# Kernel optimization log

Measured on AMD Instinct MI355X. Metric: run time of the kernel, lower is better.

## Reference

```python
import jax, jax.numpy as jnp
import numpy as np

DM = 1024
H = 16
DEPTH = DM // H


def setup_inputs() -> dict:
    key = jax.random.key(0)
    ks = jax.random.split(key, 11)
    B, S = 2, 2048
    scale = 1.0 / np.sqrt(DM)
    inp = {
        "Q": jax.random.normal(ks[0], (B, S, DM), dtype=jnp.float32),
        "K": jax.random.normal(ks[1], (B, S, DM), dtype=jnp.float32),
        "V": jax.random.normal(ks[2], (B, S, DM), dtype=jnp.float32),
        "Wq": jax.random.normal(ks[3], (DM, DM), dtype=jnp.float32) * scale,
        "bq": jnp.zeros((DM,), dtype=jnp.float32),
        "Wk": jax.random.normal(ks[4], (DM, DM), dtype=jnp.float32) * scale,
        "bk": jnp.zeros((DM,), dtype=jnp.float32),
        "Wv": jax.random.normal(ks[5], (DM, DM), dtype=jnp.float32) * scale,
        "bv": jnp.zeros((DM,), dtype=jnp.float32),
        "Wo": jax.random.normal(ks[6], (DM, DM), dtype=jnp.float32) * scale,
        "bo": jnp.zeros((DM,), dtype=jnp.float32),
    }
    return inp


def _split_heads(x, B):
    # [B, S, DM] -> [B, H, S, DEPTH]
    return x.reshape(B, -1, H, DEPTH).transpose(0, 2, 1, 3)


def reference(Q, K, V, Wq, bq, Wk, bk, Wv, bv, Wo, bo):
    B = Q.shape[0]
    q = _split_heads(Q @ Wq + bq, B)  # [B,H,S,D]
    k = _split_heads(K @ Wk + bk, B)
    v = _split_heads(V @ Wv + bv, B)
    logits = jnp.einsum("bhqd,bhkd->bhqk", q, k) / jnp.sqrt(
        jnp.asarray(DEPTH, dtype=q.dtype))
    weights = jax.nn.softmax(logits, axis=-1)  # [B,H,S,S]
    attn = jnp.einsum("bhqk,bhkd->bhqd", weights, v)
    concat = attn.transpose(0, 2, 1, 3).reshape(B, -1, DM)
    output = concat @ Wo + bo
    return output, weights
```

## Files before the change

kernel.cpp:

```cpp
#include <hip/hip_runtime.h>
#include <hip/hip_fp16.h>
#include <stdint.h>
#include <stddef.h>

typedef _Float16 f16;
typedef _Float16 f16x8 __attribute__((ext_vector_type(8)));
typedef _Float16 f16x4 __attribute__((ext_vector_type(4)));
typedef float    f32x4 __attribute__((ext_vector_type(4)));

#define NB  2
#define NS  2048
#define NDM 1024
#define NH  16
#define ND  64
#define NM  4096

__global__ __launch_bounds__(256) void cvt_x_kernel(const float* __restrict__ q,
                                                    const float* __restrict__ k,
                                                    const float* __restrict__ v,
                                                    f16* __restrict__ xh)
{
    const float* src = (blockIdx.y == 0) ? q : (blockIdx.y == 1) ? k : v;
    f16* dst = xh + (size_t)blockIdx.y * ((size_t)NM * NDM);
    size_t i = ((size_t)blockIdx.x * 256 + threadIdx.x) * 8;
    float4 a = *(const float4*)(src + i);
    float4 b = *(const float4*)(src + i + 4);
    f16x8 o;
    o[0] = (f16)a.x; o[1] = (f16)a.y; o[2] = (f16)a.z; o[3] = (f16)a.w;
    o[4] = (f16)b.x; o[5] = (f16)b.y; o[6] = (f16)b.z; o[7] = (f16)b.w;
    *(f16x8*)(dst + i) = o;
}

__global__ __launch_bounds__(256) void transp_w_kernel(const float* __restrict__ w0,
                                                       const float* __restrict__ w1,
                                                       const float* __restrict__ w2,
                                                       const float* __restrict__ w3,
                                                       f16* __restrict__ wt)
{
    __shared__ float t[64][65];
    const int z = blockIdx.z;
    const float* src = (z==0)?w0:(z==1)?w1:(z==2)?w2:w3;
    f16* dst = wt + (size_t)z * ((size_t)NDM * NDM);
    const int k0 = blockIdx.y * 64, n0 = blockIdx.x * 64;
    const int c = threadIdx.x & 63, r4 = threadIdx.x >> 6;
    #pragma unroll
    for (int i = 0; i < 16; ++i) {
        int r = i*4 + r4;
        t[r][c] = src[(size_t)(k0 + r) * NDM + n0 + c];
    }
    __syncthreads();
    #pragma unroll
    for (int i = 0; i < 16; ++i) {
        int n = i*4 + r4;
        dst[(size_t)(n0 + n) * NDM + k0 + c] = (f16)t[c][n];
    }
}

template<int MODE>
__device__ __forceinline__ void gemm128(const f16* __restrict__ A,
                                        const f16* __restrict__ Bw,
                                        const float* __restrict__ bias,
                                        void* __restrict__ outp,
                                        f16* __restrict__ AsB, f16* __restrict__ BsB)
{
    const int tid  = threadIdx.x;
    const int lane = tid & 63;
    const int wid  = tid >> 6;
    const int wr = wid >> 1, wc = wid & 1;
    const int m0 = blockIdx.y * 128, n0 = blockIdx.x * 128;
    const int K = 1024;

    const int r0 = tid >> 2;
    const int s0 = (tid & 3) * 8;
    const f16* Arow0 = A  + (size_t)(m0 + r0)      * K + s0;
    const f16* Arow1 = A  + (size_t)(m0 + r0 + 64) * K + s0;
    const f16* Brow0 = Bw + (size_t)(n0 + r0)      * K + s0;
    const f16* Brow1 = Bw + (size_t)(n0 + r0 + 64) * K + s0;
    const int lds0 = r0*32 + s0;
    const int lds1 = (r0+64)*32 + s0;

    f16x8 ra0 = *(const f16x8*)(Arow0);
    f16x8 ra1 = *(const f16x8*)(Arow1);
    f16x8 rb0 = *(const f16x8*)(Brow0);
    f16x8 rb1 = *(const f16x8*)(Brow1);
    *(f16x8*)(AsB + lds0) = ra0; *(f16x8*)(AsB + lds1) = ra1;
    *(f16x8*)(BsB + lds0) = rb0; *(f16x8*)(BsB + lds1) = rb1;

    f32x4 acc[4][4];
    #pragma unroll
    for (int i = 0; i < 4; ++i)
        #pragma unroll
        for (int j = 0; j < 4; ++j) {
            f32x4 z4 = {0.f, 0.f, 0.f, 0.f};
            acc[i][j] = z4;
        }

    const int arow = wr*64 + (lane & 15);
    const int brow = wc*64 + (lane & 15);
    const int kc   = (lane >> 4) * 8;

    int cur = 0;
    for (int s = 0; s < 32; ++s) {
        const bool more = (s + 1 < 32);
        if (more) {
            const int kk = (s + 1) * 32;
            ra0 = *(const f16x8*)(Arow0 + kk); ra1 = *(const f16x8*)(Arow1 + kk);
            rb0 = *(const f16x8*)(Brow0 + kk); rb1 = *(const f16x8*)(Brow1 + kk);
        }
        __syncthreads();
        {
            f16x8 af[4], bf[4];
            f16* Asc = AsB + cur*4096;
            f16* Bsc = BsB + cur*4096;
            #pragma unroll
            for (int rt = 0; rt < 4; ++rt) af[rt] = *(const f16x8*)(Asc + (arow + rt*16)*32 + kc);
            #pragma unroll
            for (int ct = 0; ct < 4; ++ct) bf[ct] = *(const f16x8*)(Bsc + (brow + ct*16)*32 + kc);
            #pragma unroll
            for (int rt = 0; rt < 4; ++rt)
                #pragma unroll
                for (int ct = 0; ct < 4; ++ct)
                    acc[rt][ct] = __builtin_amdgcn_mfma_f32_16x16x32_f16(af[rt], bf[ct], acc[rt][ct], 0, 0, 0);
        }
        __syncthreads();
        if (more) {
            f16* Asn = AsB + (cur^1)*4096;
            f16* Bsn = BsB + (cur^1)*4096;
            *(f16x8*)(Asn + lds0) = ra0; *(f16x8*)(Asn + lds1) = ra1;
            *(f16x8*)(Bsn + lds0) = rb0; *(f16x8*)(Bsn + lds1) = rb1;
        }
        cur ^= 1;
    }

    #pragma unroll
    for (int rt = 0; rt < 4; ++rt) {
        const int mb = m0 + wr*64 + rt*16 + ((lane >> 4) << 2);
        #pragma unroll
        for (int ct = 0; ct < 4; ++ct) {
            const int n = n0 + wc*64 + ct*16 + (lane & 15);
            const float bn = bias[n];
            if (MODE == 0 || MODE == 1) {
                f16* dst = (f16*)outp;
                const float sc = (MODE == 0) ? 0.125f : 1.0f;
                #pragma unroll
                for (int j = 0; j < 4; ++j) {
                    const int m = mb + j;
                    const float v = (acc[rt][ct][j] + bn) * sc;
                    dst[(size_t)((m >> 11)*16 + (n >> 6))*131072 + (size_t)(m & 2047)*64 + (n & 63)] = (f16)v;
                }
            } else if (MODE == 2) {
                f16* dst = (f16*)outp;
                f16x4 o;
                #pragma unroll
                for (int j = 0; j < 4; ++j) o[j] = (f16)(acc[rt][ct][j] + bn);
                *(f16x4*)(dst + (size_t)((mb >> 11)*16 + (n >> 6))*131072 + (size_t)(n & 63)*2048 + (mb & 2047)) = o;
            } else {
                float* dst = (float*)outp;
                #pragma unroll
                for (int j = 0; j < 4; ++j) {
                    const int m = mb + j;
                    dst[(size_t)m * NDM + n] = acc[rt][ct][j] + bn;
                }
            }
        }
    }
}

__global__ __launch_bounds__(256) void proj_kernel(const f16* __restrict__ xh, const f16* __restrict__ wt,
                                                   const float* __restrict__ bq, const float* __restrict__ bk,
                                                   const float* __restrict__ bv,
                                                   f16* __restrict__ qh, f16* __restrict__ kh, f16* __restrict__ vh)
{
    __shared__ f16 AsS[2*4096];
    __shared__ f16 BsS[2*4096];
    const int z = blockIdx.z;
    const f16* A  = xh + (size_t)z * ((size_t)NM * NDM);
    const f16* Bw = wt + (size_t)z * ((size_t)NDM * NDM);
    if (z == 0)      gemm128<0>(A, Bw, bq, qh, AsS, BsS);
    else if (z == 1) gemm128<1>(A, Bw, bk, kh, AsS, BsS);
    else             gemm128<2>(A, Bw, bv, vh, AsS, BsS);
}

__global__ __launch_bounds__(256) void outproj_kernel(const f16* __restrict__ ah, const f16* __restrict__ wto,
                                                      const float* __restrict__ bo, float* __restrict__ out)
{
    __shared__ f16 AsS[2*4096];
    __shared__ f16 BsS[2*4096];
    gemm128<3>(ah, wto, bo, out, AsS, BsS);
}

__global__ __launch_bounds__(512) void attn_kernel(const f16* __restrict__ qh, const f16* __restrict__ kh,
                                                   const f16* __restrict__ vt, f16* __restrict__ ah,
                                                   float* __restrict__ wout)
{
    __shared__ f16   st[16 * 2056];
    __shared__ float scratch[2048];
    __shared__ float rinv[16];

    const int tid  = threadIdx.x;
    const int lane = tid & 63;
    const int wid  = tid >> 6;

    const int xcd   = blockIdx.x & 7;
    const int j     = blockIdx.x >> 3;
    const int bh    = xcd * 4 + (j & 3);
    const int qbase = (j >> 2) * 16;

    const f16* qp = qh + ((size_t)bh * NS + qbase) * 64;
    const f16* kp = kh + (size_t)bh * NS * 64;
    const f16* vp = vt + (size_t)bh * 64 * NS;

    const int l15 = lane & 15;
    const int g   = lane >> 4;

    const f16x8 qf0 = *(const f16x8*)(qp + l15*64 + g*8);
    const f16x8 qf1 = *(const f16x8*)(qp + l15*64 + 32 + g*8);

    float rs = 0.f;
    const f16* kbase = kp + (size_t)(wid*16 + l15) * 64 + g*8;
    f16* stw = st + l15*2056 + wid*16 + g*4;

    for (int t = 0; t < 16; ++t) {
        const f16* kb = kbase + (size_t)t * (128*64);
        f16x8 kf0 = *(const f16x8*)(kb);
        f16x8 kf1 = *(const f16x8*)(kb + 32);
        f32x4 a = {0.f, 0.f, 0.f, 0.f};
        a = __builtin_amdgcn_mfma_f32_16x16x32_f16(kf0, qf0, a, 0, 0, 0);
        a = __builtin_amdgcn_mfma_f32_16x16x32_f16(kf1, qf1, a, 0, 0, 0);
        f16x4 sv;
        #pragma unroll
        for (int j2 = 0; j2 < 4; ++j2) {
            float e = __expf(a[j2]);
            e = fminf(e, 60000.0f);
            rs += e;
            sv[j2] = (f16)e;
        }
        *(f16x4*)(stw + t*128) = sv;
    }

    rs += __shfl_xor(rs, 16);
    rs += __shfl_xor(rs, 32);
    if (lane < 16) scratch[wid*16 + lane] = rs;
    __syncthreads();
    if (tid < 16) {
        float sum = 0.f;
        #pragma unroll
        for (int w = 0; w < 8; ++w) sum += scratch[w*16 + tid];
        rinv[tid] = 1.0f / sum;
    }
    __syncthreads();

    {
        const int r = tid >> 5, c = tid & 31;
        const float ri = rinv[r];
        const f16x4* srow = (const f16x4*)(st + r*2056);
        float* orow = wout + ((size_t)bh * NS + qbase + r) * NS;
        #pragma unroll
        for (int i = 0; i < 16; ++i) {
            f16x4 sv = srow[c + i*32];
            f32x4 o;
            o[0] = (float)sv[0] * ri; o[1] = (float)sv[1] * ri;
            o[2] = (float)sv[2] * ri; o[3] = (float)sv[3] * ri;
            __builtin_nontemporal_store(o, (f32x4*)(orow + (size_t)(c + i*32)*4));
        }
    }

    {
        const int nt = wid & 3;
        const int khalf = wid >> 2;
        f32x4 acc = {0.f, 0.f, 0.f, 0.f};
        const f16* vb = vp + (size_t)(nt*16 + l15) * NS + khalf*1024 + g*8;
        const f16* sb = st + l15*2056 + khalf*1024 + g*8;
        #pragma unroll 4
        for (int ks = 0; ks < 32; ++ks) {
            f16x8 sf = *(const f16x8*)(sb + ks*32);
            f16x8 vf = *(const f16x8*)(vb + ks*32);
            acc = __builtin_amdgcn_mfma_f32_16x16x32_f16(sf, vf, acc, 0, 0, 0);
        }
        #pragma unroll
        for (int j2 = 0; j2 < 4; ++j2)
            scratch[khalf*1024 + (g*4 + j2)*64 + nt*16 + l15] = acc[j2];
    }
    __syncthreads();

    {
        const int b = bh >> 4, hh = bh & 15;
        for (int idx = tid; idx < 1024; idx += 512) {
            const int r = idx >> 6, d = idx & 63;
            const float v = (scratch[r*64 + d] + scratch[1024 + r*64 + d]) * rinv[r];
            ah[((size_t)(b*NS + qbase + r)) * NDM + hh*64 + d] = (f16)v;
        }
    }
}

extern "C" void kernel_launch(void* const* d_in, const int* in_sizes, int n_in,
                              void* d_out, int out_size, void* d_ws, size_t ws_size,
                              hipStream_t stream)
{
    (void)in_sizes; (void)n_in; (void)out_size;
    const float* Q  = (const float*)d_in[0];
    const float* K  = (const float*)d_in[1];
    const float* V  = (const float*)d_in[2];
    const float* Wq = (const float*)d_in[3];
    const float* bq = (const float*)d_in[4];
    const float* Wk = (const float*)d_in[5];
    const float* bk = (const float*)d_in[6];
    const float* Wv = (const float*)d_in[7];
    const float* bv = (const float*)d_in[8];
    const float* Wo = (const float*)d_in[9];
    const float* bo = (const float*)d_in[10];

    if (ws_size < 67108864ull) return;

    f16* ws = (f16*)d_ws;
    f16* Xh = ws;
    f16* Wt = ws + 12582912;
    f16* qh = ws + 16777216;
    f16* kh = ws + 20971520;
    f16* vt = ws + 25165824;
    f16* ah = ws + 29360128;
    float* out  = (float*)d_out;
    float* wout = out + 4194304;

    cvt_x_kernel  <<<dim3(2048, 3, 1), dim3(256), 0, stream>>>(Q, K, V, Xh);
    transp_w_kernel<<<dim3(16, 16, 4), dim3(256), 0, stream>>>(Wq, Wk, Wv, Wo, Wt);
    proj_kernel   <<<dim3(8, 32, 3),  dim3(256), 0, stream>>>(Xh, Wt, bq, bk, bv, qh, kh, vt);
    attn_kernel   <<<dim3(4096),      dim3(512), 0, stream>>>(qh, kh, vt, ah, wout);
    outproj_kernel<<<dim3(8, 32, 1),  dim3(256), 0, stream>>>(ah, Wt + 3*1048576, bo, out);
}
```

Baseline: 350.9 us.

## Specialize attention warps into store and PV groups, use exp2 with folded log2e

```diff
diff --git a/kernel.cpp b/kernel.cpp
--- a/kernel.cpp
+++ b/kernel.cpp
@@ -141,7 +141,7 @@
             const float bn = bias[n];
             if (MODE == 0 || MODE == 1) {
                 f16* dst = (f16*)outp;
-                const float sc = (MODE == 0) ? 0.125f : 1.0f;
+                const float sc = (MODE == 0) ? 0.125f * 1.44269504088896f : 1.0f;
                 #pragma unroll
                 for (int j = 0; j < 4; ++j) {
                     const int m = mb + j;
@@ -194,7 +194,7 @@
                                                    float* __restrict__ wout)
 {
     __shared__ f16   st[16 * 2056];
-    __shared__ float scratch[2048];
+    __shared__ float redbuf[128];
     __shared__ float rinv[16];
 
     const int tid  = threadIdx.x;
@@ -229,67 +229,56 @@
         a = __builtin_amdgcn_mfma_f32_16x16x32_f16(kf1, qf1, a, 0, 0, 0);
         f16x4 sv;
         #pragma unroll
-        for (int j2 = 0; j2 < 4; ++j2) {
-            float e = __expf(a[j2]);
-            e = fminf(e, 60000.0f);
+        for (int u = 0; u < 4; ++u) {
+            float e = __builtin_amdgcn_exp2f(a[u]);
             rs += e;
-            sv[j2] = (f16)e;
+            sv[u] = (f16)e;
         }
         *(f16x4*)(stw + t*128) = sv;
     }
 
     rs += __shfl_xor(rs, 16);
     rs += __shfl_xor(rs, 32);
-    if (lane < 16) scratch[wid*16 + lane] = rs;
+    if (lane < 16) redbuf[wid*16 + lane] = rs;
     __syncthreads();
     if (tid < 16) {
         float sum = 0.f;
         #pragma unroll
-        for (int w = 0; w < 8; ++w) sum += scratch[w*16 + tid];
+        for (int w = 0; w < 8; ++w) sum += redbuf[w*16 + tid];
         rinv[tid] = 1.0f / sum;
     }
     __syncthreads();
 
-    {
-        const int r = tid >> 5, c = tid & 31;
+    if (wid < 4) {
+        const int r = wid*4 + g;
         const float ri = rinv[r];
         const f16x4* srow = (const f16x4*)(st + r*2056);
         float* orow = wout + ((size_t)bh * NS + qbase + r) * NS;
-        #pragma unroll
-        for (int i = 0; i < 16; ++i) {
-            f16x4 sv = srow[c + i*32];
+        #pragma unroll 8
+        for (int i = 0; i < 32; ++i) {
+            f16x4 sv = srow[l15 + i*16];
             f32x4 o;
             o[0] = (float)sv[0] * ri; o[1] = (float)sv[1] * ri;
             o[2] = (float)sv[2] * ri; o[3] = (float)sv[3] * ri;
-            __builtin_nontemporal_store(o, (f32x4*)(orow + (size_t)(c + i*32)*4));
-        }
-    }
-
-    {
-        const int nt = wid & 3;
-        const int khalf = wid >> 2;
+            __builtin_nontemporal_store(o, (f32x4*)(orow + (size_t)(l15 + i*16)*4));
+        }
+    } else {
+        const int nt = wid - 4;
         f32x4 acc = {0.f, 0.f, 0.f, 0.f};
-        const f16* vb = vp + (size_t)(nt*16 + l15) * NS + khalf*1024 + g*8;
-        const f16* sb = st + l15*2056 + khalf*1024 + g*8;
-        #pragma unroll 4
-        for (int ks = 0; ks < 32; ++ks) {
+        const f16* vb = vp + (size_t)(nt*16 + l15) * NS + g*8;
+        const f16* sb = st + l15*2056 + g*8;
+        #pragma unroll 8
+        for (int ks = 0; ks < 64; ++ks) {
+            f16x8 vf = *(const f16x8*)(vb + ks*32);
             f16x8 sf = *(const f16x8*)(sb + ks*32);
-            f16x8 vf = *(const f16x8*)(vb + ks*32);
-            acc = __builtin_amdgcn_mfma_f32_16x16x32_f16(sf, vf, acc, 0, 0, 0);
-        }
-        #pragma unroll
-        for (int j2 = 0; j2 < 4; ++j2)
-            scratch[khalf*1024 + (g*4 + j2)*64 + nt*16 + l15] = acc[j2];
-    }
-    __syncthreads();
-
-    {
-        const int b = bh >> 4, hh = bh & 15;
-        for (int idx = tid; idx < 1024; idx += 512) {
-            const int r = idx >> 6, d = idx & 63;
-            const float v = (scratch[r*64 + d] + scratch[1024 + r*64 + d]) * rinv[r];
-            ah[((size_t)(b*NS + qbase + r)) * NDM + hh*64 + d] = (f16)v;
-        }
+            acc = __builtin_amdgcn_mfma_f32_16x16x32_f16(vf, sf, acc, 0, 0, 0);
+        }
+        const float ri = rinv[l15];
+        const int bb = bh >> 4, hh = bh & 15;
+        f16x4 o;
+        #pragma unroll
+        for (int u = 0; u < 4; ++u) o[u] = (f16)(acc[u] * ri);
+        *(f16x4*)(ah + ((size_t)(bb*NS + qbase + l15)) * NDM + hh*64 + nt*16 + g*4) = o;
     }
 }
 
```

Result: no change. 357.0 us (+1.7%).

## Split attention-weight writeout into separate recompute kernel and use exp2

Applied to the files above, without the earlier changes.

```diff
diff --git a/kernel.cpp b/kernel.cpp
--- a/kernel.cpp
+++ b/kernel.cpp
@@ -141,7 +141,7 @@
             const float bn = bias[n];
             if (MODE == 0 || MODE == 1) {
                 f16* dst = (f16*)outp;
-                const float sc = (MODE == 0) ? 0.125f : 1.0f;
+                const float sc = (MODE == 0) ? 0.125f * 1.44269504088896f : 1.0f;
                 #pragma unroll
                 for (int j = 0; j < 4; ++j) {
                     const int m = mb + j;
@@ -191,7 +191,7 @@
 
 __global__ __launch_bounds__(512) void attn_kernel(const f16* __restrict__ qh, const f16* __restrict__ kh,
                                                    const f16* __restrict__ vt, f16* __restrict__ ah,
-                                                   float* __restrict__ wout)
+                                                   float* __restrict__ rws)
 {
     __shared__ f16   st[16 * 2056];
     __shared__ float scratch[2048];
@@ -204,7 +204,8 @@
     const int xcd   = blockIdx.x & 7;
     const int j     = blockIdx.x >> 3;
     const int bh    = xcd * 4 + (j & 3);
-    const int qbase = (j >> 2) * 16;
+    const int qt    = j >> 2;
+    const int qbase = qt * 16;
 
     const f16* qp = qh + ((size_t)bh * NS + qbase) * 64;
     const f16* kp = kh + (size_t)bh * NS * 64;
@@ -229,11 +230,10 @@
         a = __builtin_amdgcn_mfma_f32_16x16x32_f16(kf1, qf1, a, 0, 0, 0);
         f16x4 sv;
         #pragma unroll
-        for (int j2 = 0; j2 < 4; ++j2) {
-            float e = __expf(a[j2]);
-            e = fminf(e, 60000.0f);
+        for (int u = 0; u < 4; ++u) {
+            float e = __builtin_amdgcn_exp2f(a[u]);
             rs += e;
-            sv[j2] = (f16)e;
+            sv[u] = (f16)e;
         }
         *(f16x4*)(stw + t*128) = sv;
     }
@@ -246,24 +246,11 @@
         float sum = 0.f;
         #pragma unroll
         for (int w = 0; w < 8; ++w) sum += scratch[w*16 + tid];
-        rinv[tid] = 1.0f / sum;
-    }
-    __syncthreads();
-
-    {
-        const int r = tid >> 5, c = tid & 31;
-        const float ri = rinv[r];
-        const f16x4* srow = (const f16x4*)(st + r*2056);
-        float* orow = wout + ((size_t)bh * NS + qbase + r) * NS;
-        #pragma unroll
-        for (int i = 0; i < 16; ++i) {
-            f16x4 sv = srow[c + i*32];
-            f32x4 o;
-            o[0] = (float)sv[0] * ri; o[1] = (float)sv[1] * ri;
-            o[2] = (float)sv[2] * ri; o[3] = (float)sv[3] * ri;
-            __builtin_nontemporal_store(o, (f32x4*)(orow + (size_t)(c + i*32)*4));
-        }
-    }
+        const float r_ = 1.0f / sum;
+        rinv[tid] = r_;
+        rws[((size_t)bh * 128 + qt) * 16 + tid] = r_;
+    }
+    __syncthreads();
 
     {
         const int nt = wid & 3;
@@ -278,8 +265,8 @@
             acc = __builtin_amdgcn_mfma_f32_16x16x32_f16(sf, vf, acc, 0, 0, 0);
         }
         #pragma unroll
-        for (int j2 = 0; j2 < 4; ++j2)
-            scratch[khalf*1024 + (g*4 + j2)*64 + nt*16 + l15] = acc[j2];
+        for (int u = 0; u < 4; ++u)
+            scratch[khalf*1024 + (g*4 + u)*64 + nt*16 + l15] = acc[u];
     }
     __syncthreads();
 
@@ -289,6 +276,69 @@
             const int r = idx >> 6, d = idx & 63;
             const float v = (scratch[r*64 + d] + scratch[1024 + r*64 + d]) * rinv[r];
             ah[((size_t)(b*NS + qbase + r)) * NDM + hh*64 + d] = (f16)v;
+        }
+    }
+}
+
+__global__ __launch_bounds__(512) void wstream_kernel(const f16* __restrict__ qh,
+                                                      const f16* __restrict__ kh,
+                                                      const float* __restrict__ rws,
+                                                      float* __restrict__ wout)
+{
+    __shared__ f16 st[16 * 1032];
+
+    const int tid  = threadIdx.x;
+    const int lane = tid & 63;
+    const int wid  = tid >> 6;
+    const int l15  = lane & 15;
+    const int g    = lane >> 4;
+
+    const int xcd  = blockIdx.x & 7;
+    const int j    = blockIdx.x >> 3;
+    const int bh   = xcd * 4 + (j & 3);
+    const int rest = j >> 2;
+    const int qt   = rest >> 1;
+    const int kh2  = rest & 1;
+    const int qbase = qt * 16;
+    const int kbase = kh2 * 1024;
+
+    const f16* qp = qh + ((size_t)bh * NS + qbase) * 64;
+    const f16x8 qf0 = *(const f16x8*)(qp + l15*64 + g*8);
+    const f16x8 qf1 = *(const f16x8*)(qp + l15*64 + 32 + g*8);
+
+    const f16* kp = kh + (size_t)bh * NS * 64;
+    const f16* kb0 = kp + (size_t)(kbase + wid*16 + l15) * 64 + g*8;
+    f16* stw = st + l15*1032 + wid*16 + g*4;
+
+    #pragma unroll
+    for (int t = 0; t < 8; ++t) {
+        const f16* kb = kb0 + (size_t)t * (128*64);
+        f16x8 kf0 = *(const f16x8*)(kb);
+        f16x8 kf1 = *(const f16x8*)(kb + 32);
+        f32x4 a = {0.f, 0.f, 0.f, 0.f};
+        a = __builtin_amdgcn_mfma_f32_16x16x32_f16(kf0, qf0, a, 0, 0, 0);
+        a = __builtin_amdgcn_mfma_f32_16x16x32_f16(kf1, qf1, a, 0, 0, 0);
+        f16x4 sv;
+        #pragma unroll
+        for (int u = 0; u < 4; ++u) sv[u] = (f16)__builtin_amdgcn_exp2f(a[u]);
+        *(f16x4*)(stw + t*128) = sv;
+    }
+    __syncthreads();
+
+    const size_t rbase = ((size_t)bh * 128 + qt) * 16;
+    #pragma unroll
+    for (int rr = 0; rr < 2; ++rr) {
+        const int r = wid*2 + rr;
+        const float ri = rws[rbase + r];
+        const f16* srow = st + r*1032;
+        float* orow = wout + ((size_t)bh * NS + qbase + r) * NS + kbase;
+        #pragma unroll
+        for (int i = 0; i < 4; ++i) {
+            f16x4 sv = *(const f16x4*)(srow + i*256 + lane*4);
+            f32x4 o;
+            o[0] = (float)sv[0] * ri; o[1] = (float)sv[1] * ri;
+            o[2] = (float)sv[2] * ri; o[3] = (float)sv[3] * ri;
+            __builtin_nontemporal_store(o, (f32x4*)(orow + i*256 + lane*4));
         }
     }
 }
@@ -319,12 +369,14 @@
     f16* kh = ws + 20971520;
     f16* vt = ws + 25165824;
     f16* ah = ws + 29360128;
+    float* rws = (float*)ws;
     float* out  = (float*)d_out;
     float* wout = out + 4194304;
 
     cvt_x_kernel  <<<dim3(2048, 3, 1), dim3(256), 0, stream>>>(Q, K, V, Xh);
     transp_w_kernel<<<dim3(16, 16, 4), dim3(256), 0, stream>>>(Wq, Wk, Wv, Wo, Wt);
     proj_kernel   <<<dim3(8, 32, 3),  dim3(256), 0, stream>>>(Xh, Wt, bq, bk, bv, qh, kh, vt);
-    attn_kernel   <<<dim3(4096),      dim3(512), 0, stream>>>(qh, kh, vt, ah, wout);
+    attn_kernel   <<<dim3(4096),      dim3(512), 0, stream>>>(qh, kh, vt, ah, rws);
+    wstream_kernel<<<dim3(8192),      dim3(512), 0, stream>>>(qh, kh, rws, wout);
     outproj_kernel<<<dim3(8, 32, 1),  dim3(256), 0, stream>>>(ah, Wt + 3*1048576, bo, out);
 }
```

Result: slower. 477.4 us (+36.0%).
